# Kernel tuning notes

Measured on AMD Instinct MI355X. Metric: run time of the kernel, lower is better.

Reference implementation:

```python
import jax, jax.numpy as jnp
import numpy as np

FEAT_DIM = 48        # feature_dim init arg
C_OUT = 2 * FEAT_DIM # conv output channels -> table row width
H = W_IMG = 256      # image spatial size -> res = C_OUT*H*W / (2*FEAT_DIM) = 65536
N_PTS = 2_000_000    # query points


def setup_inputs() -> dict:
    key = jax.random.key(0)
    k1, k2, k3, k4 = jax.random.split(key, 4)
    pts = jax.random.uniform(k1, (N_PTS, 2), dtype=jnp.float32)  # coords in [0,1)
    image = jax.random.normal(k2, (1, 3, H, W_IMG), dtype=jnp.float32)
    conv_w = jax.random.normal(k3, (C_OUT, 3, 3, 3), dtype=jnp.float32) * 0.05
    conv_b = jax.random.normal(k4, (C_OUT,), dtype=jnp.float32) * 0.05
    return {"pts": pts, "image": image, "conv_w": conv_w, "conv_b": conv_b}


def reference(pts, image, conv_w, conv_b):
    # feature_extractor: Conv2d(3, 96, k=3, SAME) -> [1, 96, 256, 256]
    feat = jax.lax.conv_general_dilated(
        image, conv_w, window_strides=(1, 1), padding="SAME",
        dimension_numbers=("NCHW", "OIHW", "NCHW"))
    feat = feat + conv_b[None, :, None, None]
    fa = feat.reshape(-1, 2 * FEAT_DIM)  # [res, 96]
    res = fa.shape[0]                    # 65536

    x = pts[:, 0] * (res - 1)
    y = pts[:, 1] * (res - 1)
    hi = res - 1 - 1e-5
    x1 = jnp.floor(jnp.clip(x, 0, hi)).astype(jnp.int32)
    y1 = jnp.floor(jnp.clip(y, 0, hi)).astype(jnp.int32)
    x2 = jnp.clip(x1 + 1, 0, res - 1)
    y2 = jnp.clip(y1 + 1, 0, res - 1)

    xw1 = (x2.astype(x.dtype) - x)[:, None]
    xw2 = (x - x1.astype(x.dtype))[:, None]
    yw1 = (y2.astype(y.dtype) - y)[:, None]
    yw2 = (y - y1.astype(y.dtype))[:, None]

    fx = fa[:, :FEAT_DIM]  # x-array half of the dual array
    fy = fa[:, FEAT_DIM:]  # y-array half
    # four gathers + weighted blend -> [N, FEAT_DIM]
    return xw1 * fx[x1] + xw2 * fx[x2] + yw1 * fy[y1] + yw2 * fy[y2]
```

## Files before the change

kernel.cpp:

```cpp
#include <hip/hip_runtime.h>
#include <hip/hip_bf16.h>

#define C_OUT 96
#define FEAT_DIM 48
#define HW 256
#define NPIX 65536
#define RES 65536
#define IMG_C 3
#define NBUCKET 256
#define SCAT_PPT 8

typedef __attribute__((ext_vector_type(2))) float f32x2;
typedef __attribute__((ext_vector_type(4))) float f32x4;
typedef __attribute__((ext_vector_type(8))) unsigned short u16x8;
typedef __attribute__((ext_vector_type(4))) unsigned short u16x4;

static __device__ __forceinline__ unsigned short f2bf(float f) {
    unsigned u = __float_as_uint(f);
    u += 0x7fffu + ((u >> 16) & 1u);
    return (unsigned short)(u >> 16);
}
static __device__ __forceinline__ float bf2f(unsigned short h) {
    return __uint_as_float(((unsigned)h) << 16);
}
static __device__ __forceinline__ float clipcoord(float p) {
    return fminf(fmaxf(p * 65535.0f, 0.0f), 65535.0f);
}
static __device__ __forceinline__ int bkey(float x, float y) {
    int x1 = (int)x, y1 = (int)y;
    return ((x1 >> 12) << 4) | (y1 >> 12);
}

__global__ __launch_bounds__(256) void conv_kernel(
    const float* __restrict__ img, const float* __restrict__ w,
    const float* __restrict__ b,
    unsigned short* __restrict__ FX, unsigned short* __restrict__ FY)
{
    __shared__ float ws[C_OUT * 27];
    __shared__ float bs[C_OUT];
    for (int i = threadIdx.x; i < C_OUT * 27; i += blockDim.x) ws[i] = w[i];
    for (int i = threadIdx.x; i < C_OUT; i += blockDim.x) bs[i] = b[i];
    __syncthreads();

    int tid = blockIdx.x * blockDim.x + threadIdx.x;
    if (tid >= (C_OUT * NPIX) / 4) return;
    int f = tid << 2;
    int c  = f >> 16;
    int p  = f & 65535;
    int h  = p >> 8;
    int wc = p & 255;

    float a0 = bs[c], a1 = a0, a2 = a0, a3 = a0;
#pragma unroll
    for (int ci = 0; ci < IMG_C; ++ci) {
        const float* ip = img + ci * NPIX;
#pragma unroll
        for (int kh = 0; kh < 3; ++kh) {
            int hh = h + kh - 1;
            if ((unsigned)hh >= 256u) continue;
            const float* row = ip + hh * HW;
            float win[6];
#pragma unroll
            for (int k = 0; k < 6; ++k) {
                int ww = wc + k - 1;
                win[k] = ((unsigned)ww < 256u) ? row[ww] : 0.0f;
            }
            const float* wk = &ws[c * 27 + ci * 9 + kh * 3];
#pragma unroll
            for (int kw = 0; kw < 3; ++kw) {
                float wt = wk[kw];
                a0 = fmaf(win[kw + 0], wt, a0);
                a1 = fmaf(win[kw + 1], wt, a1);
                a2 = fmaf(win[kw + 2], wt, a2);
                a3 = fmaf(win[kw + 3], wt, a3);
            }
        }
    }

    int r = (unsigned)f / 96u;
    int j = f - r * 96;
    u16x4 pk;
    pk.x = f2bf(a0); pk.y = f2bf(a1); pk.z = f2bf(a2); pk.w = f2bf(a3);
    unsigned short* dst = (j < FEAT_DIM)
        ? (FX + (size_t)r * FEAT_DIM + j)
        : (FY + (size_t)r * FEAT_DIM + (j - FEAT_DIM));
    *(u16x4*)dst = pk;
}

__global__ __launch_bounds__(256) void hist_kernel(
    const float* __restrict__ pts, unsigned* __restrict__ hist, int npts)
{
    __shared__ unsigned lh[NBUCKET];
    for (int i = threadIdx.x; i < NBUCKET; i += blockDim.x) lh[i] = 0;
    __syncthreads();
    int stride = gridDim.x * blockDim.x;
    for (int i = blockIdx.x * blockDim.x + threadIdx.x; i < npts; i += stride) {
        f32x2 p = *((const f32x2*)pts + i);
        atomicAdd(&lh[bkey(clipcoord(p.x), clipcoord(p.y))], 1u);
    }
    __syncthreads();
    for (int i = threadIdx.x; i < NBUCKET; i += blockDim.x)
        if (lh[i]) atomicAdd(&hist[i], lh[i]);
}

__global__ __launch_bounds__(256) void scan_kernel(
    const unsigned* __restrict__ hist, unsigned* __restrict__ cursor)
{
    __shared__ unsigned tmp[NBUCKET];
    int t = threadIdx.x;
    unsigned own = hist[t];
    tmp[t] = own;
    __syncthreads();
#pragma unroll
    for (int off = 1; off < NBUCKET; off <<= 1) {
        unsigned v = (t >= off) ? tmp[t - off] : 0u;
        __syncthreads();
        tmp[t] += v;
        __syncthreads();
    }
    cursor[t] = tmp[t] - own;
}

__global__ __launch_bounds__(256) void scatter_kernel(
    const float* __restrict__ pts, unsigned* __restrict__ cursor,
    f32x4* __restrict__ sorted, int npts)
{
    __shared__ unsigned lh[NBUCKET];
    __shared__ unsigned lbase[NBUCKET];
    int t = threadIdx.x;
    for (int i = t; i < NBUCKET; i += blockDim.x) lh[i] = 0;
    __syncthreads();

    int start = blockIdx.x * (blockDim.x * SCAT_PPT);
    float xs[SCAT_PPT], ys[SCAT_PPT];
    int keys[SCAT_PPT];
#pragma unroll
    for (int k = 0; k < SCAT_PPT; ++k) {
        int i = start + k * blockDim.x + t;
        if (i < npts) {
            f32x2 p = *((const f32x2*)pts + i);
            xs[k] = clipcoord(p.x);
            ys[k] = clipcoord(p.y);
            keys[k] = bkey(xs[k], ys[k]);
            atomicAdd(&lh[keys[k]], 1u);
        } else keys[k] = -1;
    }
    __syncthreads();
    for (int i = t; i < NBUCKET; i += blockDim.x)
        lbase[i] = lh[i] ? atomicAdd(&cursor[i], lh[i]) : 0u;
    __syncthreads();
    for (int i = t; i < NBUCKET; i += blockDim.x) lh[i] = 0;
    __syncthreads();
#pragma unroll
    for (int k = 0; k < SCAT_PPT; ++k) {
        if (keys[k] >= 0) {
            unsigned slot = lbase[keys[k]] + atomicAdd(&lh[keys[k]], 1u);
            int i = start + k * blockDim.x + t;
            f32x4 rec;
            rec.x = xs[k]; rec.y = ys[k];
            rec.z = __uint_as_float((unsigned)i); rec.w = 0.0f;
            sorted[slot] = rec;
        }
    }
}

__global__ __launch_bounds__(256) void interp_kernel(
    const f32x4* __restrict__ sorted,
    const unsigned short* __restrict__ FX,
    const unsigned short* __restrict__ FY,
    float* __restrict__ out, int npts, int nblk)
{
    int orig = blockIdx.x;
    int xcd = orig & 7;
    int q8 = nblk >> 3, r8 = nblk & 7;
    int base = (xcd < r8) ? xcd * (q8 + 1) : r8 * (q8 + 1) + (xcd - r8) * q8;
    int sbid = base + (orig >> 3);

    int t = sbid * blockDim.x + threadIdx.x;
    int s = t / 6;
    int q = t - s * 6;
    if (s >= npts) return;

    f32x4 rec = sorted[s];
    float x = rec.x, y = rec.y;
    unsigned idx = __float_as_uint(rec.z);

    int x1 = (int)x;
    int y1 = (int)y;
    int x2 = min(x1 + 1, RES - 1);
    int y2 = min(y1 + 1, RES - 1);

    float xw1 = (float)x2 - x;
    float xw2 = x - (float)x1;
    float yw1 = (float)y2 - y;
    float yw2 = y - (float)y1;

    int qo = q * 8;
    const u16x8 A = *(const u16x8*)(FX + (size_t)x1 * FEAT_DIM + qo);
    const u16x8 B = *(const u16x8*)(FX + (size_t)x2 * FEAT_DIM + qo);
    const u16x8 C = *(const u16x8*)(FY + (size_t)y1 * FEAT_DIM + qo);
    const u16x8 D = *(const u16x8*)(FY + (size_t)y2 * FEAT_DIM + qo);

    float o[8];
#pragma unroll
    for (int k = 0; k < 8; ++k) {
        o[k] = xw1 * bf2f(A[k]) + xw2 * bf2f(B[k])
             + yw1 * bf2f(C[k]) + yw2 * bf2f(D[k]);
    }

    float* op = out + (size_t)idx * FEAT_DIM + qo;
    f32x4 v0 = {o[0], o[1], o[2], o[3]};
    f32x4 v1 = {o[4], o[5], o[6], o[7]};
    __builtin_nontemporal_store(v0, (f32x4*)op);
    __builtin_nontemporal_store(v1, (f32x4*)(op + 4));
}

extern "C" void kernel_launch(void* const* d_in, const int* in_sizes, int n_in,
                              void* d_out, int out_size, void* d_ws, size_t ws_size,
                              hipStream_t stream) {
    const float* pts    = (const float*)d_in[0];
    const float* image  = (const float*)d_in[1];
    const float* conv_w = (const float*)d_in[2];
    const float* conv_b = (const float*)d_in[3];
    float* out = (float*)d_out;

    int npts = in_sizes[0] / 2;

    char* wsb = (char*)d_ws;
    f32x4* sorted = (f32x4*)wsb;
    size_t sorted_bytes = ((size_t)npts * 16 + 255) & ~(size_t)255;
    unsigned short* FX = (unsigned short*)(wsb + sorted_bytes);
    unsigned short* FY = FX + (size_t)RES * FEAT_DIM;
    unsigned* hist   = (unsigned*)(wsb + sorted_bytes + 2 * (size_t)RES * FEAT_DIM * 2);
    unsigned* cursor = hist + NBUCKET;

    hipMemsetAsync(hist, 0, NBUCKET * sizeof(unsigned), stream);

    {
        int total = (C_OUT * NPIX) / 4;
        conv_kernel<<<(total + 255) / 256, 256, 0, stream>>>(image, conv_w, conv_b, FX, FY);
    }
    hist_kernel<<<1024, 256, 0, stream>>>(pts, hist, npts);
    scan_kernel<<<1, 256, 0, stream>>>(hist, cursor);
    {
        int per_block = 256 * SCAT_PPT;
        int blocks = (npts + per_block - 1) / per_block;
        scatter_kernel<<<blocks, 256, 0, stream>>>(pts, cursor, sorted, npts);
    }
    {
        long long total = (long long)npts * 6;
        int nblk = (int)((total + 255) / 256);
        interp_kernel<<<nblk, 256, 0, stream>>>(sorted, FX, FY, out, npts, nblk);
    }
}
```

Measured before the change: 236.2 us.

## Split point sort into index windows and run interp per window

Bucketing now uses a coarser 8x8 spatial grid combined with two windows over the original point index. Interpolation runs as one launch per window, so each launch's output writes land in a contiguous half of the output array and can stay cache-resident. The nontemporal stores become regular stores to exploit that. The trade-off is coarser spatial sorting, which may weaken gather locality in the feature tables, plus an extra kernel launch.

Result: slower. 260.1 us (+10.1%).

```diff
diff --git a/kernel.cpp b/kernel.cpp
--- a/kernel.cpp
+++ b/kernel.cpp
@@ -7,7 +7,11 @@
 #define NPIX 65536
 #define RES 65536
 #define IMG_C 3
-#define NBUCKET 256
+#define NKX 8
+#define NKY 8
+#define NKEY_W (NKX * NKY)
+#define NWIN 2
+#define NKEY (NKEY_W * NWIN)
 #define SCAT_PPT 8
 
 typedef __attribute__((ext_vector_type(2))) float f32x2;
@@ -26,9 +30,8 @@
 static __device__ __forceinline__ float clipcoord(float p) {
     return fminf(fmaxf(p * 65535.0f, 0.0f), 65535.0f);
 }
-static __device__ __forceinline__ int bkey(float x, float y) {
-    int x1 = (int)x, y1 = (int)y;
-    return ((x1 >> 12) << 4) | (y1 >> 12);
+static __device__ __forceinline__ int bucket_of(float x, float y) {
+    return (((int)x >> 13) << 3) | ((int)y >> 13);
 }
 
 __global__ __launch_bounds__(256) void conv_kernel(
@@ -88,47 +91,50 @@
 }
 
 __global__ __launch_bounds__(256) void hist_kernel(
-    const float* __restrict__ pts, unsigned* __restrict__ hist, int npts)
-{
-    __shared__ unsigned lh[NBUCKET];
-    for (int i = threadIdx.x; i < NBUCKET; i += blockDim.x) lh[i] = 0;
+    const float* __restrict__ pts, unsigned* __restrict__ hist,
+    int npts, int wsize)
+{
+    __shared__ unsigned lh[NKEY];
+    for (int i = threadIdx.x; i < NKEY; i += blockDim.x) lh[i] = 0;
     __syncthreads();
     int stride = gridDim.x * blockDim.x;
     for (int i = blockIdx.x * blockDim.x + threadIdx.x; i < npts; i += stride) {
         f32x2 p = *((const f32x2*)pts + i);
-        atomicAdd(&lh[bkey(clipcoord(p.x), clipcoord(p.y))], 1u);
-    }
-    __syncthreads();
-    for (int i = threadIdx.x; i < NBUCKET; i += blockDim.x)
+        int key = (i / wsize) * NKEY_W + bucket_of(clipcoord(p.x), clipcoord(p.y));
+        atomicAdd(&lh[key], 1u);
+    }
+    __syncthreads();
+    for (int i = threadIdx.x; i < NKEY; i += blockDim.x)
         if (lh[i]) atomicAdd(&hist[i], lh[i]);
 }
 
 __global__ __launch_bounds__(256) void scan_kernel(
     const unsigned* __restrict__ hist, unsigned* __restrict__ cursor)
 {
-    __shared__ unsigned tmp[NBUCKET];
+    __shared__ unsigned tmp[NKEY];
     int t = threadIdx.x;
-    unsigned own = hist[t];
-    tmp[t] = own;
-    __syncthreads();
-#pragma unroll
-    for (int off = 1; off < NBUCKET; off <<= 1) {
-        unsigned v = (t >= off) ? tmp[t - off] : 0u;
+    unsigned own = 0;
+    if (t < NKEY) { own = hist[t]; tmp[t] = own; }
+    __syncthreads();
+#pragma unroll
+    for (int off = 1; off < NKEY; off <<= 1) {
+        unsigned v = 0;
+        if (t < NKEY && t >= off) v = tmp[t - off];
         __syncthreads();
-        tmp[t] += v;
+        if (t < NKEY) tmp[t] += v;
         __syncthreads();
     }
-    cursor[t] = tmp[t] - own;
+    if (t < NKEY) cursor[t] = tmp[t] - own;
 }
 
 __global__ __launch_bounds__(256) void scatter_kernel(
     const float* __restrict__ pts, unsigned* __restrict__ cursor,
-    f32x4* __restrict__ sorted, int npts)
-{
-    __shared__ unsigned lh[NBUCKET];
-    __shared__ unsigned lbase[NBUCKET];
+    f32x4* __restrict__ sorted, int npts, int wsize)
+{
+    __shared__ unsigned lh[NKEY];
+    __shared__ unsigned lbase[NKEY];
     int t = threadIdx.x;
-    for (int i = t; i < NBUCKET; i += blockDim.x) lh[i] = 0;
+    for (int i = t; i < NKEY; i += blockDim.x) lh[i] = 0;
     __syncthreads();
 
     int start = blockIdx.x * (blockDim.x * SCAT_PPT);
@@ -141,15 +147,15 @@
             f32x2 p = *((const f32x2*)pts + i);
             xs[k] = clipcoord(p.x);
             ys[k] = clipcoord(p.y);
-            keys[k] = bkey(xs[k], ys[k]);
+            keys[k] = (i / wsize) * NKEY_W + bucket_of(xs[k], ys[k]);
             atomicAdd(&lh[keys[k]], 1u);
         } else keys[k] = -1;
     }
     __syncthreads();
-    for (int i = t; i < NBUCKET; i += blockDim.x)
+    for (int i = t; i < NKEY; i += blockDim.x)
         lbase[i] = lh[i] ? atomicAdd(&cursor[i], lh[i]) : 0u;
     __syncthreads();
-    for (int i = t; i < NBUCKET; i += blockDim.x) lh[i] = 0;
+    for (int i = t; i < NKEY; i += blockDim.x) lh[i] = 0;
     __syncthreads();
 #pragma unroll
     for (int k = 0; k < SCAT_PPT; ++k) {
@@ -168,20 +174,20 @@
     const f32x4* __restrict__ sorted,
     const unsigned short* __restrict__ FX,
     const unsigned short* __restrict__ FY,
-    float* __restrict__ out, int npts, int nblk)
+    float* __restrict__ out, int base, int count, int nblk)
 {
     int orig = blockIdx.x;
     int xcd = orig & 7;
     int q8 = nblk >> 3, r8 = nblk & 7;
-    int base = (xcd < r8) ? xcd * (q8 + 1) : r8 * (q8 + 1) + (xcd - r8) * q8;
-    int sbid = base + (orig >> 3);
+    int cbase = (xcd < r8) ? xcd * (q8 + 1) : r8 * (q8 + 1) + (xcd - r8) * q8;
+    int sbid = cbase + (orig >> 3);
 
     int t = sbid * blockDim.x + threadIdx.x;
     int s = t / 6;
     int q = t - s * 6;
-    if (s >= npts) return;
-
-    f32x4 rec = sorted[s];
+    if (s >= count) return;
+
+    f32x4 rec = sorted[base + s];
     float x = rec.x, y = rec.y;
     unsigned idx = __float_as_uint(rec.z);
 
@@ -211,8 +217,8 @@
     float* op = out + (size_t)idx * FEAT_DIM + qo;
     f32x4 v0 = {o[0], o[1], o[2], o[3]};
     f32x4 v1 = {o[4], o[5], o[6], o[7]};
-    __builtin_nontemporal_store(v0, (f32x4*)op);
-    __builtin_nontemporal_store(v1, (f32x4*)(op + 4));
+    *(f32x4*)op = v0;
+    *(f32x4*)(op + 4) = v1;
 }
 
 extern "C" void kernel_launch(void* const* d_in, const int* in_sizes, int n_in,
@@ -225,6 +231,7 @@
     float* out = (float*)d_out;
 
     int npts = in_sizes[0] / 2;
+    int wsize = (npts + NWIN - 1) / NWIN;
 
     char* wsb = (char*)d_ws;
     f32x4* sorted = (f32x4*)wsb;
@@ -232,24 +239,27 @@
     unsigned short* FX = (unsigned short*)(wsb + sorted_bytes);
     unsigned short* FY = FX + (size_t)RES * FEAT_DIM;
     unsigned* hist   = (unsigned*)(wsb + sorted_bytes + 2 * (size_t)RES * FEAT_DIM * 2);
-    unsigned* cursor = hist + NBUCKET;
-
-    hipMemsetAsync(hist, 0, NBUCKET * sizeof(unsigned), stream);
+    unsigned* cursor = hist + NKEY;
+
+    hipMemsetAsync(hist, 0, NKEY * sizeof(unsigned), stream);
 
     {
         int total = (C_OUT * NPIX) / 4;
         conv_kernel<<<(total + 255) / 256, 256, 0, stream>>>(image, conv_w, conv_b, FX, FY);
     }
-    hist_kernel<<<1024, 256, 0, stream>>>(pts, hist, npts);
+    hist_kernel<<<1024, 256, 0, stream>>>(pts, hist, npts, wsize);
     scan_kernel<<<1, 256, 0, stream>>>(hist, cursor);
     {
         int per_block = 256 * SCAT_PPT;
         int blocks = (npts + per_block - 1) / per_block;
-        scatter_kernel<<<blocks, 256, 0, stream>>>(pts, cursor, sorted, npts);
-    }
-    {
-        long long total = (long long)npts * 6;
-        int nblk = (int)((total + 255) / 256);
-        interp_kernel<<<nblk, 256, 0, stream>>>(sorted, FX, FY, out, npts, nblk);
-    }
-}
+        scatter_kernel<<<blocks, 256, 0, stream>>>(pts, cursor, sorted, npts, wsize);
+    }
+    for (int wdx = 0; wdx < NWIN; ++wdx) {
+        int base = wdx * wsize;
+        int count = (base < npts) ? min(wsize, npts - base) : 0;
+        if (count <= 0) break;
+        long long lanes = (long long)count * 6;
+        int nblk = (int)((lanes + 255) / 256);
+        interp_kernel<<<nblk, 256, 0, stream>>>(sorted, FX, FY, out, base, count, nblk);
+    }
+}
```
